# Kernel tuning notes

Measured on AMD Instinct MI355X. Metric: run time of the kernel, lower is better.

The kernel has to match this reference:

```python
import jax, jax.numpy as jnp
import numpy as np

B, T, DEMO = 64, 4096, 8
N_MOD, N_POS = 37, 10
D_IN = N_POS + 1 + N_MOD  # 48
PHI_W, LATENT = 128, 128
PSI_W, PSI_L = 128, 128
DOT, HEADS = 64, 4
RHO_W, OUT = 128, 1
MAX_TIME = 1000.0


def _dense_init(key, fan_in, fan_out):
    lim = float(np.sqrt(6.0 / fan_in))  # he_uniform-ish
    return jax.random.uniform(key, (fan_in, fan_out), jnp.float32, -lim, lim)


def setup_inputs() -> dict:
    key = jax.random.key(0)
    ks = jax.random.split(key, 32)
    inp = {}
    inp['demo'] = jax.random.normal(ks[0], (B, DEMO), jnp.float32)
    inp['times'] = jax.random.uniform(ks[1], (B, T, 1), jnp.float32, 0.0, 100.0)
    inp['values'] = jax.random.normal(ks[2], (B, T, 1), jnp.float32)
    inp['measurements'] = jax.random.randint(ks[3], (B, T), 0, N_MOD, jnp.int32)
    # all sequences full length -> N = B*(T+1) static
    inp['segment_ids'] = jnp.repeat(jnp.arange(B, dtype=jnp.int32), T + 1)
    inp['timescales'] = jnp.asarray(MAX_TIME ** np.linspace(0.0, 1.0, N_POS // 2), jnp.float32)
    inp['demo_W1'] = _dense_init(ks[4], DEMO, PHI_W); inp['demo_b1'] = jnp.zeros((PHI_W,), jnp.float32)
    inp['demo_W2'] = _dense_init(ks[5], PHI_W, D_IN); inp['demo_b2'] = jnp.zeros((D_IN,), jnp.float32)
    dims = [D_IN, PHI_W, PHI_W, PHI_W, LATENT]
    for i in range(4):
        inp['phi_W%d' % i] = _dense_init(ks[6 + i], dims[i], dims[i + 1])
        inp['phi_b%d' % i] = jnp.zeros((dims[i + 1],), jnp.float32)
    pdims = [D_IN, PSI_W, PSI_W, PSI_L]
    for i in range(3):
        inp['psi_W%d' % i] = _dense_init(ks[10 + i], pdims[i], pdims[i + 1])
        inp['psi_b%d' % i] = jnp.zeros((pdims[i + 1],), jnp.float32)
    inp['W_k'] = _dense_init(ks[13], PSI_L + D_IN, DOT * HEADS)
    # original inits W_q to zeros (degenerate uniform attention); small random keeps test non-trivial
    inp['W_q'] = jax.random.normal(ks[14], (HEADS, DOT), jnp.float32) * 0.05
    rdims = [LATENT * HEADS, RHO_W, RHO_W, RHO_W, OUT]
    for i in range(4):
        inp['rho_W%d' % i] = _dense_init(ks[15 + i], rdims[i], rdims[i + 1])
        inp['rho_b%d' % i] = jnp.zeros((rdims[i + 1],), jnp.float32)
    return inp


def _forward(demo, times, values, timescales,
             demo_W1, demo_b1, demo_W2, demo_b2,
             phi_W0, phi_b0, phi_W1, phi_b1, phi_W2, phi_b2, phi_W3, phi_b3,
             psi_W0, psi_b0, psi_W1, psi_b1, psi_W2, psi_b2,
             W_k, W_q,
             rho_W0, rho_b0, rho_W1, rho_b1, rho_W2, rho_b2, rho_W3, rho_b3,
             measurements, segment_ids):
    relu = jax.nn.relu
    nseg = demo.shape[0]
    # positional encoding: times [B,T,1] / timescales [5] -> sin|cos -> [B,T,10]
    scaled = times / timescales[None, None, :]
    tt = jnp.concatenate([jnp.sin(scaled), jnp.cos(scaled)], axis=-1)
    meas = jax.nn.one_hot(measurements, N_MOD, dtype=times.dtype)  # [B,T,37]
    combined = jnp.concatenate([tt, values, meas], axis=-1)        # [B,T,48]
    demo_enc = relu(demo @ demo_W1 + demo_b1) @ demo_W2 + demo_b2  # [B,48]
    x = jnp.concatenate([demo_enc[:, None, :], combined], axis=1)  # [B,T+1,48]
    collected = x.reshape(-1, x.shape[-1])                         # [N,48]
    # phi MLP -> encoded [N,LATENT]
    h = collected
    for W, b in ((phi_W0, phi_b0), (phi_W1, phi_b1), (phi_W2, phi_b2), (phi_W3, phi_b3)):
        h = relu(h @ W + b)
    encoded = h
    # psi MLP -> [N,PSI_L], then per-segment mean, scattered back
    p = collected
    for W, b in ((psi_W0, psi_b0), (psi_W1, psi_b1), (psi_W2, psi_b2)):
        p = relu(p @ W + b)
    seg_sum = jax.ops.segment_sum(p, segment_ids, num_segments=nseg)
    counts = jax.ops.segment_sum(jnp.ones((p.shape[0],), p.dtype), segment_ids, num_segments=nseg)
    agg = seg_sum / counts[:, None]
    comb2 = jnp.concatenate([collected, agg[segment_ids]], axis=-1)  # [N, 48+128]
    keys = (comb2 @ W_k).reshape(-1, HEADS, DOT)                     # [N,H,D]
    preattn = jnp.einsum('nhd,hd->nh', keys, W_q) / jnp.sqrt(jnp.float32(DOT))
    # segment softmax per head
    m = jax.ops.segment_max(preattn, segment_ids, num_segments=nseg)
    e = jnp.exp(preattn - m[segment_ids])
    s = jax.ops.segment_sum(e, segment_ids, num_segments=nseg)
    attn = e / s[segment_ids]                                        # [N,H]
    # head-major weighted concat: [N, H*LATENT]
    weighted = (attn[:, :, None] * encoded[:, None, :]).reshape(-1, HEADS * LATENT)
    agg_out = jax.ops.segment_sum(weighted, segment_ids, num_segments=nseg)  # [B,512]
    r = agg_out
    for W, b in ((rho_W0, rho_b0), (rho_W1, rho_b1), (rho_W2, rho_b2)):
        r = relu(r @ W + b)
    return jax.nn.sigmoid(r @ rho_W3 + rho_b3)  # [B,1]


def reference(demo, times, values, timescales,
              demo_W1, demo_b1, demo_W2, demo_b2,
              phi_W0, phi_b0, phi_W1, phi_b1, phi_W2, phi_b2, phi_W3, phi_b3,
              psi_W0, psi_b0, psi_W1, psi_b1, psi_W2, psi_b2,
              W_k, W_q,
              rho_W0, rho_b0, rho_W1, rho_b1, rho_W2, rho_b2, rho_W3, rho_b3,
              measurements, segment_ids):
    return _forward(demo, times, values, timescales,
                    demo_W1, demo_b1, demo_W2, demo_b2,
                    phi_W0, phi_b0, phi_W1, phi_b1, phi_W2, phi_b2, phi_W3, phi_b3,
                    psi_W0, psi_b0, psi_W1, psi_b1, psi_W2, psi_b2,
                    W_k, W_q,
                    rho_W0, rho_b0, rho_W1, rho_b1, rho_W2, rho_b2, rho_W3, rho_b3,
                    measurements, segment_ids)
```

## Files before the change

### kernel.cpp

```cpp
#include <hip/hip_runtime.h>
#include <hip/hip_bf16.h>
#include <math.h>


#define BSEG 64
#define TLEN 4096
#define NPART 9
#define PART_STRIDE 520

#define OFF_DEMO 0
#define OFF_WQ   3072
#define OFF_WT   3264
#define OFF_PARTIALS 31936

typedef __attribute__((ext_vector_type(8))) short short8;
typedef __attribute__((ext_vector_type(4))) float f32x4;

static __device__ __forceinline__ float bfbits2f(unsigned v) { return __uint_as_float(v << 16); }
static __device__ __forceinline__ unsigned short f2bf_rne(float x) {
  unsigned u = __float_as_uint(x);
  unsigned r = (u + 0x7FFFu + ((u >> 16) & 1u)) >> 16;
  return (unsigned short)r;
}
static __device__ __forceinline__ unsigned pk2(float a, float b) {
  float2 f2 = make_float2(a, b);
  __hip_bfloat162 h = __float22bfloat162_rn(f2);
  unsigned u;
  __builtin_memcpy(&u, &h, 4);
  return u;
}

__global__ __launch_bounds__(256) void k_prep(
    const float* __restrict__ demo, const float* __restrict__ dW1, const float* __restrict__ db1,
    const float* __restrict__ dW2, const float* __restrict__ db2,
    const float* __restrict__ Wk, const float* __restrict__ Wq,
    const float* __restrict__ W0, const float* __restrict__ W1,
    const float* __restrict__ W2, const float* __restrict__ W3,
    float* __restrict__ ws) {
  __shared__ float drow[8];
  __shared__ float hdrow[128];
  int bid = blockIdx.x, tid = threadIdx.x;
  if (bid < 224) {
    unsigned short* wt = (unsigned short*)(ws + OFF_WT);
    int i = bid * 256 + tid;
    float v;
    if (i < 8192) {
      int n = i >> 6, k = i & 63;
      v = (k < 48) ? W0[k * 128 + n] : 0.f;
    } else {
      int j = i - 8192;
      int l = j >> 14, r = j & 16383;
      int n = r >> 7, k = r & 127;
      const float* W = (l == 0) ? W1 : (l == 1) ? W2 : W3;
      v = W[k * 128 + n];
    }
    wt[i] = f2bf_rne(v);
    return;
  }
  if (bid == 224) {
    if (tid < 192) {
      int i = tid >> 2, h = tid & 3;
      float a = 0.f;
      for (int d = 0; d < 64; ++d) a = fmaf(Wk[i * 256 + h * 64 + d], Wq[h * 64 + d], a);
      ws[OFF_WQ + tid] = a * 0.125f;
    }
    return;
  }
  int r = bid - 225;
  if (tid < 8) drow[tid] = demo[r * 8 + tid];
  __syncthreads();
  if (tid < 128) {
    float a = db1[tid];
#pragma unroll
    for (int i = 0; i < 8; ++i) a = fmaf(drow[i], dW1[i * 128 + tid], a);
    hdrow[tid] = fmaxf(a, 0.f);
  }
  __syncthreads();
  if (tid < 48) {
    float a = db2[tid];
    for (int k = 0; k < 128; ++k) a = fmaf(hdrow[k], dW2[k * 48 + tid], a);
    ws[OFF_DEMO + r * 48 + tid] = a;
  }
}

template<int MT>
static __device__ __forceinline__ void mfma_layer_T(
    const unsigned short* hin, unsigned short* hout,
    const short8 (&Wf)[2][4], const f32x4 (&bias4)[2],
    int l16, int quad, int n0) {
#pragma unroll
  for (int mt = 0; mt < MT; ++mt) {
    short8 Bv[4];
#pragma unroll
    for (int s = 0; s < 4; ++s)
      Bv[s] = *(const short8*)(hin + (mt * 16 + l16) * 136 + s * 32 + quad * 8);
#pragma unroll
    for (int t = 0; t < 2; ++t) {
      f32x4 acc = bias4[t];
#pragma unroll
      for (int s = 0; s < 4; ++s)
        acc = __builtin_amdgcn_mfma_f32_16x16x32_bf16(Wf[t][s], Bv[s], acc, 0, 0, 0);
      unsigned u01 = pk2(fmaxf(acc[0], 0.f), fmaxf(acc[1], 0.f));
      unsigned u23 = pk2(fmaxf(acc[2], 0.f), fmaxf(acc[3], 0.f));
      *(uint2*)(hout + (mt * 16 + l16) * 136 + n0 + t * 16 + quad * 4) =
          make_uint2(u01, u23);
    }
  }
}
template<int MT>
static __device__ __forceinline__ void mfma_layer0_T(
    const unsigned short* cin, unsigned short* hout,
    const short8 (&Wf)[2][2], const f32x4 (&bias4)[2],
    int l16, int quad, int n0) {
#pragma unroll
  for (int mt = 0; mt < MT; ++mt) {
    short8 Bv[2];
#pragma unroll
    for (int s = 0; s < 2; ++s)
      Bv[s] = *(const short8*)(cin + (mt * 16 + l16) * 72 + s * 32 + quad * 8);
#pragma unroll
    for (int t = 0; t < 2; ++t) {
      f32x4 acc = bias4[t];
      acc = __builtin_amdgcn_mfma_f32_16x16x32_bf16(Wf[t][0], Bv[0], acc, 0, 0, 0);
      acc = __builtin_amdgcn_mfma_f32_16x16x32_bf16(Wf[t][1], Bv[1], acc, 0, 0, 0);
      unsigned u01 = pk2(fmaxf(acc[0], 0.f), fmaxf(acc[1], 0.f));
      unsigned u23 = pk2(fmaxf(acc[2], 0.f), fmaxf(acc[3], 0.f));
      *(uint2*)(hout + (mt * 16 + l16) * 136 + n0 + t * 16 + quad * 4) =
          make_uint2(u01, u23);
    }
  }
}

__global__ __launch_bounds__(256, 2) void k_main(
    const float* __restrict__ times, const float* __restrict__ values,
    const int* __restrict__ meas, const float* __restrict__ tsc,
    const float* __restrict__ ws,
    const float* __restrict__ b0g, const float* __restrict__ b1g,
    const float* __restrict__ b2g, const float* __restrict__ b3g,
    float* __restrict__ part) {
  __shared__ __align__(16) unsigned short hA[128 * 136];
  __shared__ __align__(16) unsigned short hB[128 * 136];
  __shared__ __align__(16) float preb[512 * 4];
  __shared__ float wql[192];
  __shared__ float mred[16];
  int tid = threadIdx.x;
  const int lane = tid & 63, wv = tid >> 6, quad = lane >> 4, l16 = lane & 15;
  const int n0 = wv * 32;

  const unsigned short* wt = (const unsigned short*)(ws + OFF_WT);
  short8 B0[2][2], B1[2][4], B2[2][4], B3[2][4];
  f32x4 bias0[2], bias1[2], bias2[2];
  float bias3[2];
#pragma unroll
  for (int t = 0; t < 2; ++t) {
    int n = n0 + t * 16 + l16;
    int nq = n0 + t * 16 + quad * 4;
    bias0[t] = *(const f32x4*)(b0g + nq);
    bias1[t] = *(const f32x4*)(b1g + nq);
    bias2[t] = *(const f32x4*)(b2g + nq);
    bias3[t] = b3g[n];
#pragma unroll
    for (int s = 0; s < 2; ++s)
      B0[t][s] = *(const short8*)(wt + n * 64 + s * 32 + quad * 8);
#pragma unroll
    for (int s = 0; s < 4; ++s) {
      B1[t][s] = *(const short8*)(wt + 8192  + n * 128 + s * 32 + quad * 8);
      B2[t][s] = *(const short8*)(wt + 24576 + n * 128 + s * 32 + quad * 8);
      B3[t][s] = *(const short8*)(wt + 40960 + n * 128 + s * 32 + quad * 8);
    }
  }
  if (tid < 192) wql[tid] = ws[OFF_WQ + tid];
  __syncthreads();

  if (blockIdx.x == 512) {
    {
      int r = tid >> 2, cs = tid & 3;
      unsigned short seg[16];
#pragma unroll
      for (int i = 0; i < 16; ++i) seg[i] = 0;
      if (cs < 3)
#pragma unroll
        for (int i = 0; i < 16; ++i) seg[i] = f2bf_rne(ws[OFF_DEMO + r * 48 + cs * 16 + i]);
      unsigned u[8];
#pragma unroll
      for (int i = 0; i < 8; ++i) u[i] = (unsigned)seg[2 * i] | ((unsigned)seg[2 * i + 1] << 16);
      uint4* dst = (uint4*)(hB + r * 72 + cs * 16);
      dst[0] = make_uint4(u[0], u[1], u[2], u[3]);
      dst[1] = make_uint4(u[4], u[5], u[6], u[7]);
    }
    {
      int r = tid >> 2, h = tid & 3;
      float a = 0.f;
      for (int i = 0; i < 48; ++i) a = fmaf(ws[OFF_DEMO + r * 48 + i], wql[i * 4 + h], a);
      preb[tid] = __expf(a);
    }
    f32x4 bias34[2];
#pragma unroll
    for (int t = 0; t < 2; ++t) bias34[t] = *(const f32x4*)(b3g + n0 + t * 16 + quad * 4);
    __syncthreads();
    mfma_layer0_T<4>(hB, hA, B0, bias0, l16, quad, n0); __syncthreads();
    mfma_layer_T<4>(hA, hB, B1, bias1, l16, quad, n0); __syncthreads();
    mfma_layer_T<4>(hB, hA, B2, bias2, l16, quad, n0); __syncthreads();
    mfma_layer_T<4>(hA, hB, B3, bias34, l16, quad, n0); __syncthreads();
    {
      int r = tid >> 2, h = tid & 3;
      part[(r * NPART + 8) * PART_STRIDE + 4 + h] = preb[tid];
    }
    for (int i = tid; i < 64 * 512; i += 256) {
      int r = i >> 9, rem = i & 511;
      int h = rem >> 7, l = rem & 127;
      part[(r * NPART + 8) * PART_STRIDE + 8 + rem] =
          preb[r * 4 + h] * bfbits2f(hB[r * 136 + l]);
    }
    return;
  }

  int b = blockIdx.x >> 3, c = blockIdx.x & 7;
  int t0 = c << 9;
  float invts[5];
#pragma unroll
  for (int i = 0; i < 5; ++i) invts[i] = 1.f / tsc[i];

  float s4[4] = {0.f, 0.f, 0.f, 0.f};
  for (int rr = 0; rr < 2; ++rr) {
    int r = tid + rr * 256;
    int t = t0 + r;
    float tv = times[b * TLEN + t];
    float vvv = values[b * TLEN + t];
    int mm = meas[b * TLEN + t];
    float f[11];
#pragma unroll
    for (int i = 0; i < 5; ++i) { float s = tv * invts[i]; f[i] = __sinf(s); f[5 + i] = __cosf(s); }
    f[10] = vvv;
#pragma unroll
    for (int h = 0; h < 4; ++h) {
      float a = wql[(11 + mm) * 4 + h];
#pragma unroll
      for (int i = 0; i < 11; ++i) a = fmaf(f[i], wql[i * 4 + h], a);
      float e = __expf(a);
      preb[r * 4 + h] = e;
      s4[h] += e;
    }
  }

  float pacc[2][4] = {{0.f, 0.f, 0.f, 0.f}, {0.f, 0.f, 0.f, 0.f}};
  for (int tile = 0; tile < 4; ++tile) {
    int rb = tile << 7;
    for (int ii = 0; ii < 2; ++ii) {
      int i = tid + ii * 256;
      int r = i >> 2, cs = i & 3;
      int t = t0 + rb + r;
      int mm = meas[b * TLEN + t];
      unsigned short seg[16];
#pragma unroll
      for (int k = 0; k < 16; ++k) seg[k] = 0;
      if (cs == 0) {
        float tv = times[b * TLEN + t];
        float vvv = values[b * TLEN + t];
#pragma unroll
        for (int k = 0; k < 5; ++k) {
          float s = tv * invts[k];
          seg[k] = f2bf_rne(__sinf(s));
          seg[5 + k] = f2bf_rne(__cosf(s));
        }
        seg[10] = f2bf_rne(vvv);
      }
      int kk = 11 + mm;
      if ((kk >> 4) == cs) seg[kk & 15] = 0x3F80;
      unsigned u[8];
#pragma unroll
      for (int k = 0; k < 8; ++k) u[k] = (unsigned)seg[2 * k] | ((unsigned)seg[2 * k + 1] << 16);
      uint4* dst = (uint4*)(hB + r * 72 + cs * 16);
      dst[0] = make_uint4(u[0], u[1], u[2], u[3]);
      dst[1] = make_uint4(u[4], u[5], u[6], u[7]);
    }
    __syncthreads();
    mfma_layer0_T<8>(hB, hA, B0, bias0, l16, quad, n0); __syncthreads();
    mfma_layer_T<8>(hA, hB, B1, bias1, l16, quad, n0); __syncthreads();
    mfma_layer_T<8>(hB, hA, B2, bias2, l16, quad, n0); __syncthreads();
#pragma unroll
    for (int mt = 0; mt < 8; ++mt) {
      short8 A[4];
#pragma unroll
      for (int s = 0; s < 4; ++s)
        A[s] = *(const short8*)(hA + (mt * 16 + l16) * 136 + s * 32 + quad * 8);
      f32x4 acc0 = {bias3[0], bias3[0], bias3[0], bias3[0]};
      f32x4 acc1 = {bias3[1], bias3[1], bias3[1], bias3[1]};
#pragma unroll
      for (int s = 0; s < 4; ++s) {
        acc0 = __builtin_amdgcn_mfma_f32_16x16x32_bf16(A[s], B3[0][s], acc0, 0, 0, 0);
        acc1 = __builtin_amdgcn_mfma_f32_16x16x32_bf16(A[s], B3[1][s], acc1, 0, 0, 0);
      }
#pragma unroll
      for (int j = 0; j < 4; ++j) {
        int row = rb + mt * 16 + quad * 4 + j;
        float4 e4 = *(const float4*)(preb + row * 4);
        float v0 = fmaxf(acc0[j], 0.f), v1 = fmaxf(acc1[j], 0.f);
        pacc[0][0] = fmaf(v0, e4.x, pacc[0][0]);
        pacc[0][1] = fmaf(v0, e4.y, pacc[0][1]);
        pacc[0][2] = fmaf(v0, e4.z, pacc[0][2]);
        pacc[0][3] = fmaf(v0, e4.w, pacc[0][3]);
        pacc[1][0] = fmaf(v1, e4.x, pacc[1][0]);
        pacc[1][1] = fmaf(v1, e4.y, pacc[1][1]);
        pacc[1][2] = fmaf(v1, e4.z, pacc[1][2]);
        pacc[1][3] = fmaf(v1, e4.w, pacc[1][3]);
      }
    }
  }
#pragma unroll
  for (int t = 0; t < 2; ++t)
#pragma unroll
    for (int h = 0; h < 4; ++h) {
      float v = pacc[t][h];
      v += __shfl_xor(v, 16, 64);
      v += __shfl_xor(v, 32, 64);
      pacc[t][h] = v;
    }
#pragma unroll
  for (int off = 32; off > 0; off >>= 1)
#pragma unroll
    for (int h = 0; h < 4; ++h) s4[h] += __shfl_xor(s4[h], off, 64);
  if (lane == 0)
#pragma unroll
    for (int h = 0; h < 4; ++h) mred[wv * 4 + h] = s4[h];
  __syncthreads();
  float* P = part + (b * NPART + c) * PART_STRIDE;
  if (tid < 4) P[4 + tid] = mred[tid] + mred[4 + tid] + mred[8 + tid] + mred[12 + tid];
  if (quad == 0)
#pragma unroll
    for (int t = 0; t < 2; ++t)
#pragma unroll
      for (int h = 0; h < 4; ++h)
        P[8 + h * 128 + (n0 + t * 16 + l16)] = pacc[t][h];
}

__global__ __launch_bounds__(256) void k_combine(
    const float* __restrict__ part,
    const float* __restrict__ rW0, const float* __restrict__ rb0,
    const float* __restrict__ rW1, const float* __restrict__ rb1,
    const float* __restrict__ rW2, const float* __restrict__ rb2,
    const float* __restrict__ rW3, const float* __restrict__ rb3,
    float* __restrict__ out) {
  __shared__ float Ss[4], agg[512], r1[128], p0[256];
  int tid = threadIdx.x;
  int b = blockIdx.x;
  const float* P = part + b * NPART * PART_STRIDE;
  if (tid < 4) {
    float s = 0.f;
    for (int p = 0; p < NPART; ++p) s += P[p * PART_STRIDE + 4 + tid];
    Ss[tid] = s;
  }
  __syncthreads();
  for (int idx = tid; idx < 512; idx += 256) {
    int h = idx >> 7;
    float a = 0.f;
    for (int p = 0; p < NPART; ++p) a += P[p * PART_STRIDE + 8 + idx];
    agg[idx] = a / Ss[h];
  }
  __syncthreads();
  const int col = tid & 127, half = tid >> 7;
  {
    float a = 0.f;
    for (int k = half * 256; k < half * 256 + 256; ++k) a = fmaf(agg[k], rW0[k * 128 + col], a);
    p0[tid] = a;
  }
  __syncthreads();
  if (tid < 128) r1[tid] = fmaxf(rb0[tid] + p0[tid] + p0[128 + tid], 0.f);
  __syncthreads();
  {
    float a = 0.f;
    for (int k = half * 64; k < half * 64 + 64; ++k) a = fmaf(r1[k], rW1[k * 128 + col], a);
    p0[tid] = a;
  }
  __syncthreads();
  if (tid < 128) r1[tid] = fmaxf(rb1[tid] + p0[tid] + p0[128 + tid], 0.f);
  __syncthreads();
  {
    float a = 0.f;
    for (int k = half * 64; k < half * 64 + 64; ++k) a = fmaf(r1[k], rW2[k * 128 + col], a);
    p0[tid] = a;
  }
  __syncthreads();
  if (tid < 128) p0[tid] = fmaxf(rb2[tid] + p0[tid] + p0[128 + tid], 0.f) * rW3[tid];
  __syncthreads();
  if (tid < 64) {
    float v = p0[tid] + p0[tid + 64];
#pragma unroll
    for (int off = 32; off > 0; off >>= 1) v += __shfl_xor(v, off, 64);
    if (tid == 0) out[b] = 1.f / (1.f + __expf(-(rb3[0] + v)));
  }
}

extern "C" void kernel_launch(void* const* d_in, const int* in_sizes, int n_in,
                              void* d_out, int out_size, void* d_ws, size_t ws_size,
                              hipStream_t stream) {
  const float* demo   = (const float*)d_in[0];
  const float* times  = (const float*)d_in[1];
  const float* values = (const float*)d_in[2];
  const int*   meas   = (const int*)d_in[3];
  const float* tsc = (const float*)d_in[5];
  const float* dW1 = (const float*)d_in[6];
  const float* db1 = (const float*)d_in[7];
  const float* dW2 = (const float*)d_in[8];
  const float* db2 = (const float*)d_in[9];
  const float* pW0 = (const float*)d_in[10];
  const float* pb0 = (const float*)d_in[11];
  const float* pW1 = (const float*)d_in[12];
  const float* pb1 = (const float*)d_in[13];
  const float* pW2 = (const float*)d_in[14];
  const float* pb2 = (const float*)d_in[15];
  const float* pW3 = (const float*)d_in[16];
  const float* pb3 = (const float*)d_in[17];
  const float* Wk  = (const float*)d_in[24];
  const float* Wq  = (const float*)d_in[25];
  const float* rW0 = (const float*)d_in[26];
  const float* rb0 = (const float*)d_in[27];
  const float* rW1 = (const float*)d_in[28];
  const float* rb1 = (const float*)d_in[29];
  const float* rW2 = (const float*)d_in[30];
  const float* rb2 = (const float*)d_in[31];
  const float* rW3 = (const float*)d_in[32];
  const float* rb3 = (const float*)d_in[33];
  float* ws = (float*)d_ws;
  float* partials = ws + OFF_PARTIALS;

  k_prep<<<289, 256, 0, stream>>>(demo, dW1, db1, dW2, db2, Wk, Wq,
                                  pW0, pW1, pW2, pW3, ws);
  k_main<<<513, 256, 0, stream>>>(times, values, meas, tsc, ws,
                                  pb0, pb1, pb2, pb3, partials);
  k_combine<<<64, 256, 0, stream>>>(partials, rW0, rb0, rW1, rb1, rW2, rb2, rW3, rb3,
                                    (float*)d_out);
}
```

Baseline: 184.9 us.

## Permute MLP output columns for 128-bit LDS stores and reuse computed input features

Remaps the output-neuron ordering per wave so each lane's two MFMA accumulators cover 8 contiguous columns. Each lane can then write one uint4 to LDS instead of two uint2 stores, and the bias, weight and final-output indexing are remapped to match. The sinusoidal features computed for the attention pass are packed to bf16 and kept in registers, so the per-tile input build no longer recomputes sin/cos or reloads times and values. The next tile's input is built right after layer 2, overlapping with layer 3, at the cost of more live registers.

Result: no change. 183.1 us (-1.0%).

```diff
diff --git a/kernel.cpp b/kernel.cpp
--- a/kernel.cpp
+++ b/kernel.cpp
@@ -94,17 +94,18 @@
 #pragma unroll
     for (int s = 0; s < 4; ++s)
       Bv[s] = *(const short8*)(hin + (mt * 16 + l16) * 136 + s * 32 + quad * 8);
-#pragma unroll
-    for (int t = 0; t < 2; ++t) {
-      f32x4 acc = bias4[t];
-#pragma unroll
-      for (int s = 0; s < 4; ++s)
-        acc = __builtin_amdgcn_mfma_f32_16x16x32_bf16(Wf[t][s], Bv[s], acc, 0, 0, 0);
-      unsigned u01 = pk2(fmaxf(acc[0], 0.f), fmaxf(acc[1], 0.f));
-      unsigned u23 = pk2(fmaxf(acc[2], 0.f), fmaxf(acc[3], 0.f));
-      *(uint2*)(hout + (mt * 16 + l16) * 136 + n0 + t * 16 + quad * 4) =
-          make_uint2(u01, u23);
-    }
+    f32x4 a0 = bias4[0], a1 = bias4[1];
+#pragma unroll
+    for (int s = 0; s < 4; ++s) {
+      a0 = __builtin_amdgcn_mfma_f32_16x16x32_bf16(Wf[0][s], Bv[s], a0, 0, 0, 0);
+      a1 = __builtin_amdgcn_mfma_f32_16x16x32_bf16(Wf[1][s], Bv[s], a1, 0, 0, 0);
+    }
+    uint4 o;
+    o.x = pk2(fmaxf(a0[0], 0.f), fmaxf(a0[1], 0.f));
+    o.y = pk2(fmaxf(a0[2], 0.f), fmaxf(a0[3], 0.f));
+    o.z = pk2(fmaxf(a1[0], 0.f), fmaxf(a1[1], 0.f));
+    o.w = pk2(fmaxf(a1[2], 0.f), fmaxf(a1[3], 0.f));
+    *(uint4*)(hout + (mt * 16 + l16) * 136 + n0 + quad * 8) = o;
   }
 }
 template<int MT>
@@ -118,16 +119,17 @@
 #pragma unroll
     for (int s = 0; s < 2; ++s)
       Bv[s] = *(const short8*)(cin + (mt * 16 + l16) * 72 + s * 32 + quad * 8);
-#pragma unroll
-    for (int t = 0; t < 2; ++t) {
-      f32x4 acc = bias4[t];
-      acc = __builtin_amdgcn_mfma_f32_16x16x32_bf16(Wf[t][0], Bv[0], acc, 0, 0, 0);
-      acc = __builtin_amdgcn_mfma_f32_16x16x32_bf16(Wf[t][1], Bv[1], acc, 0, 0, 0);
-      unsigned u01 = pk2(fmaxf(acc[0], 0.f), fmaxf(acc[1], 0.f));
-      unsigned u23 = pk2(fmaxf(acc[2], 0.f), fmaxf(acc[3], 0.f));
-      *(uint2*)(hout + (mt * 16 + l16) * 136 + n0 + t * 16 + quad * 4) =
-          make_uint2(u01, u23);
-    }
+    f32x4 a0 = bias4[0], a1 = bias4[1];
+    a0 = __builtin_amdgcn_mfma_f32_16x16x32_bf16(Wf[0][0], Bv[0], a0, 0, 0, 0);
+    a0 = __builtin_amdgcn_mfma_f32_16x16x32_bf16(Wf[0][1], Bv[1], a0, 0, 0, 0);
+    a1 = __builtin_amdgcn_mfma_f32_16x16x32_bf16(Wf[1][0], Bv[0], a1, 0, 0, 0);
+    a1 = __builtin_amdgcn_mfma_f32_16x16x32_bf16(Wf[1][1], Bv[1], a1, 0, 0, 0);
+    uint4 o;
+    o.x = pk2(fmaxf(a0[0], 0.f), fmaxf(a0[1], 0.f));
+    o.y = pk2(fmaxf(a0[2], 0.f), fmaxf(a0[3], 0.f));
+    o.z = pk2(fmaxf(a1[0], 0.f), fmaxf(a1[1], 0.f));
+    o.w = pk2(fmaxf(a1[2], 0.f), fmaxf(a1[3], 0.f));
+    *(uint4*)(hout + (mt * 16 + l16) * 136 + n0 + quad * 8) = o;
   }
 }
 
@@ -153,8 +155,8 @@
   float bias3[2];
 #pragma unroll
   for (int t = 0; t < 2; ++t) {
-    int n = n0 + t * 16 + l16;
-    int nq = n0 + t * 16 + quad * 4;
+    int n  = n0 + ((l16 >> 2) << 3) + t * 4 + (l16 & 3);
+    int nq = n0 + quad * 8 + t * 4;
     bias0[t] = *(const f32x4*)(b0g + nq);
     bias1[t] = *(const f32x4*)(b1g + nq);
     bias2[t] = *(const f32x4*)(b2g + nq);
@@ -196,7 +198,7 @@
     }
     f32x4 bias34[2];
 #pragma unroll
-    for (int t = 0; t < 2; ++t) bias34[t] = *(const f32x4*)(b3g + n0 + t * 16 + quad * 4);
+    for (int t = 0; t < 2; ++t) bias34[t] = *(const f32x4*)(b3g + n0 + quad * 8 + t * 4);
     __syncthreads();
     mfma_layer0_T<4>(hB, hA, B0, bias0, l16, quad, n0); __syncthreads();
     mfma_layer_T<4>(hA, hB, B1, bias1, l16, quad, n0); __syncthreads();
@@ -222,6 +224,8 @@
   for (int i = 0; i < 5; ++i) invts[i] = 1.f / tsc[i];
 
   float s4[4] = {0.f, 0.f, 0.f, 0.f};
+  unsigned usv0[8], usv1[8];
+#pragma unroll
   for (int rr = 0; rr < 2; ++rr) {
     int r = tid + rr * 256;
     int t = t0 + r;
@@ -241,43 +245,55 @@
       preb[r * 4 + h] = e;
       s4[h] += e;
     }
-  }
+    int kk = 11 + mm;
+    unsigned uu[8];
+    uu[0] = pk2(f[0], f[1]); uu[1] = pk2(f[2], f[3]);
+    uu[2] = pk2(f[4], f[5]); uu[3] = pk2(f[6], f[7]);
+    uu[4] = pk2(f[8], f[9]);
+    uu[5] = pk2(f[10], (kk == 11) ? 1.f : 0.f);
+    uu[6] = ((kk == 12) ? 0x3F80u : 0u) | ((kk == 13) ? 0x3F800000u : 0u);
+    uu[7] = ((kk == 14) ? 0x3F80u : 0u) | ((kk == 15) ? 0x3F800000u : 0u);
+    if (rr == 0) {
+#pragma unroll
+      for (int k = 0; k < 8; ++k) usv0[k] = uu[k];
+    } else {
+#pragma unroll
+      for (int k = 0; k < 8; ++k) usv1[k] = uu[k];
+    }
+  }
+
+  auto build_tile = [&](int tile) {
+    int r = tid & 127;
+    if (((tid >> 7) & 1) == (tile & 1)) {
+      unsigned uw[8];
+#pragma unroll
+      for (int k = 0; k < 8; ++k) uw[k] = (tile & 2) ? usv1[k] : usv0[k];
+      uint4* dst = (uint4*)(hB + r * 72);
+      dst[0] = make_uint4(uw[0], uw[1], uw[2], uw[3]);
+      dst[1] = make_uint4(uw[4], uw[5], uw[6], uw[7]);
+    } else {
+      int t = t0 + tile * 128 + r;
+      int mm = meas[b * TLEN + t];
+      int kk = 11 + mm;
+      uint4 z = make_uint4(0u, 0u, 0u, 0u);
+      uint4* dst = (uint4*)(hB + r * 72 + 16);
+#pragma unroll
+      for (int k = 0; k < 6; ++k) dst[k] = z;
+      asm volatile("" ::: "memory");
+      if (kk >= 16) hB[r * 72 + kk] = 0x3F80;
+    }
+  };
 
   float pacc[2][4] = {{0.f, 0.f, 0.f, 0.f}, {0.f, 0.f, 0.f, 0.f}};
+  const int ncb = n0 + ((l16 >> 2) << 3) + (l16 & 3);
+  build_tile(0);
   for (int tile = 0; tile < 4; ++tile) {
     int rb = tile << 7;
-    for (int ii = 0; ii < 2; ++ii) {
-      int i = tid + ii * 256;
-      int r = i >> 2, cs = i & 3;
-      int t = t0 + rb + r;
-      int mm = meas[b * TLEN + t];
-      unsigned short seg[16];
-#pragma unroll
-      for (int k = 0; k < 16; ++k) seg[k] = 0;
-      if (cs == 0) {
-        float tv = times[b * TLEN + t];
-        float vvv = values[b * TLEN + t];
-#pragma unroll
-        for (int k = 0; k < 5; ++k) {
-          float s = tv * invts[k];
-          seg[k] = f2bf_rne(__sinf(s));
-          seg[5 + k] = f2bf_rne(__cosf(s));
-        }
-        seg[10] = f2bf_rne(vvv);
-      }
-      int kk = 11 + mm;
-      if ((kk >> 4) == cs) seg[kk & 15] = 0x3F80;
-      unsigned u[8];
-#pragma unroll
-      for (int k = 0; k < 8; ++k) u[k] = (unsigned)seg[2 * k] | ((unsigned)seg[2 * k + 1] << 16);
-      uint4* dst = (uint4*)(hB + r * 72 + cs * 16);
-      dst[0] = make_uint4(u[0], u[1], u[2], u[3]);
-      dst[1] = make_uint4(u[4], u[5], u[6], u[7]);
-    }
     __syncthreads();
     mfma_layer0_T<8>(hB, hA, B0, bias0, l16, quad, n0); __syncthreads();
     mfma_layer_T<8>(hA, hB, B1, bias1, l16, quad, n0); __syncthreads();
     mfma_layer_T<8>(hB, hA, B2, bias2, l16, quad, n0); __syncthreads();
+    if (tile < 3) build_tile(tile + 1);
 #pragma unroll
     for (int mt = 0; mt < 8; ++mt) {
       short8 A[4];
@@ -331,7 +347,7 @@
     for (int t = 0; t < 2; ++t)
 #pragma unroll
       for (int h = 0; h < 4; ++h)
-        P[8 + h * 128 + (n0 + t * 16 + l16)] = pacc[t][h];
+        P[8 + h * 128 + (ncb + t * 4)] = pacc[t][h];
 }
 
 __global__ __launch_bounds__(256) void k_combine(
```
